# Performance work log

Hardware: AMD Instinct MI355X
Metric: run time of the kernel (lower is better)

The kernel has to match this reference:

```python
import jax, jax.numpy as jnp
import numpy as np

N_HEADS = 16
NEG_INF = -1e9


def _apply_rope(xq, xk, cos, sin):
    # xq, xk: [B, S, H, hd]; cos/sin: [S, hd//2]
    def rot(t):
        B, S, H, hd = t.shape
        t = t.reshape(B, S, H, hd // 2, 2)
        t0, t1 = t[..., 0], t[..., 1]
        c = cos[None, :, None, :]
        s = sin[None, :, None, :]
        o0 = t0 * c - t1 * s
        o1 = t0 * s + t1 * c
        return jnp.stack([o0, o1], axis=-1).reshape(B, S, H, hd)
    return rot(xq), rot(xk)


def setup_inputs() -> dict:
    key = jax.random.key(0)
    ks = jax.random.split(key, 7)
    B, S, D = 2, 2048, 2048
    hd = D // N_HEADS
    return {
        "x": jax.random.normal(ks[0], (B, S, D), dtype=jnp.float32),
        "freqs_cos": jax.random.uniform(ks[1], (S, hd // 2), dtype=jnp.float32),
        "freqs_sin": jax.random.uniform(ks[2], (S, hd // 2), dtype=jnp.float32),
        "wq": jax.random.normal(ks[3], (D, D), dtype=jnp.float32) * 0.02,
        "wk": jax.random.normal(ks[4], (D, D), dtype=jnp.float32) * 0.02,
        "wv": jax.random.normal(ks[5], (D, D), dtype=jnp.float32) * 0.02,
        "wo": jax.random.normal(ks[6], (D, D), dtype=jnp.float32) * 0.02,
    }


def reference(x, freqs_cos, freqs_sin, wq, wk, wv, wo):
    B, S, D = x.shape
    H = N_HEADS
    hd = D // H

    # projections (torch Linear: y = x @ W.T)
    xq = (x @ wq.T).reshape(B, S, H, hd)
    xk = (x @ wk.T).reshape(B, S, H, hd)
    xv = (x @ wv.T).reshape(B, S, H, hd)

    xq, xk = _apply_rope(xq, xk, freqs_cos, freqs_sin)

    # [B, H, S, hd]
    q = xq.transpose(0, 2, 1, 3)
    k = xk.transpose(0, 2, 1, 3)
    v = xv.transpose(0, 2, 1, 3)

    scores = jnp.einsum("bhqd,bhkd->bhqk", q, k) / jnp.sqrt(jnp.float32(hd))
    causal = jnp.triu(jnp.full((S, S), NEG_INF, dtype=scores.dtype), k=1)
    scores = scores + causal[None, None]
    probs = jax.nn.softmax(scores.astype(jnp.float32), axis=-1).astype(q.dtype)

    out = jnp.einsum("bhqk,bhkd->bhqd", probs, v)
    out = out.transpose(0, 2, 1, 3).reshape(B, S, D)
    return out @ wo.T
```

## Files before the change

kernel.cpp:

```cpp
#include <hip/hip_runtime.h>
#include <hip/hip_bf16.h>
#include <math.h>

typedef __attribute__((ext_vector_type(8))) short short8;
typedef __attribute__((ext_vector_type(4))) short short4v;
typedef __attribute__((ext_vector_type(4))) float f32x4;
typedef unsigned short ushort_t;

#define QK_LOG2E_SCALE 0.1275274059009601f

__device__ __forceinline__ ushort_t f2bf(float f) {
    union { float f; unsigned u; } v; v.f = f;
    unsigned r = v.u + 0x7FFF + ((v.u >> 16) & 1);
    return (ushort_t)(r >> 16);
}

__global__ void cvt_all(const float* __restrict__ x,
                        const float* __restrict__ w0, const float* __restrict__ w1,
                        const float* __restrict__ w2, const float* __restrict__ w3,
                        const float* __restrict__ fc, const float* __restrict__ fs,
                        ushort_t* __restrict__ dst, float2* __restrict__ fcs,
                        int md8, int dd8, int npair4) {
    int i = blockIdx.x * blockDim.x + threadIdx.x;
    int stride = gridDim.x * blockDim.x;
    const int total0 = md8 + 4 * dd8;
    const int total = total0 + npair4;
    for (; i < total; i += stride) {
        if (i < total0) {
            const float* src;
            long off;
            if (i < md8) { src = x; off = i; }
            else {
                int j = i - md8;
                int which = j / dd8;
                off = j - (long)which * dd8;
                src = (which == 0) ? w0 : (which == 1) ? w1 : (which == 2) ? w2 : w3;
            }
            const float4* s = reinterpret_cast<const float4*>(src) + off * 2;
            float4 a = s[0], b = s[1];
            short8 o;
            o[0] = (short)f2bf(a.x); o[1] = (short)f2bf(a.y);
            o[2] = (short)f2bf(a.z); o[3] = (short)f2bf(a.w);
            o[4] = (short)f2bf(b.x); o[5] = (short)f2bf(b.y);
            o[6] = (short)f2bf(b.z); o[7] = (short)f2bf(b.w);
            reinterpret_cast<short8*>(dst)[i] = o;
        } else {
            int j = i - total0;
            float4 c4 = reinterpret_cast<const float4*>(fc)[j];
            float4 s4 = reinterpret_cast<const float4*>(fs)[j];
            float2* o = fcs + (long)j * 4;
            o[0] = make_float2(c4.x, s4.x);
            o[1] = make_float2(c4.y, s4.y);
            o[2] = make_float2(c4.z, s4.z);
            o[3] = make_float2(c4.w, s4.w);
        }
    }
}

template<int EPI>
__global__ __launch_bounds__(512, 2) void gemm_wide(const ushort_t* __restrict__ A,
                                                    const ushort_t* __restrict__ Bw,
                                                    void* __restrict__ Cout,
                                                    ushort_t* __restrict__ Vt,
                                                    const float2* __restrict__ fcs,
                                                    int M, int N, int K) {
    extern __shared__ __align__(16) ushort_t lds[];
    ushort_t* As = lds;
    ushort_t* Bs = lds + 16384;
    const int t = threadIdx.x;
    const int wid = t >> 6, lane = t & 63;
    const int wr = wid >> 2, wc = wid & 3;
    const int lr = lane & 15, lg = lane >> 4;

    const int ntc = N >> 8;
    const int nwg = (M >> 7) * ntc;
    const int bid = blockIdx.y * gridDim.x + blockIdx.x;
    const int cpx = nwg >> 3;
    const int swz = (bid & 7) * cpx + (bid >> 3);
    const int m0 = (swz / ntc) * 128, n0 = (swz % ntc) * 256;

    f32x4 acc[4][4] = {};

    const int r0 = t >> 3;
    const int c0 = (t & 7) ^ (r0 & 7);
    const ushort_t* gA = A + (long)(m0 + r0) * K + c0 * 8;
    const ushort_t* gB = Bw + (long)(n0 + r0) * K + c0 * 8;

    int aoffE[2];
    aoffE[0] = lr * 64 + (((0 + lg) ^ (lr & 7)) << 3);
    aoffE[1] = lr * 64 + (((4 + lg) ^ (lr & 7)) << 3);

    const int nt = K >> 6;

#define STAGE_A(X) do { const int p_ = (X) & 1;                                                \
    __builtin_amdgcn_global_load_lds((const __attribute__((address_space(1))) unsigned int*)   \
        (gA + (X) * 64),                                                                       \
        (__attribute__((address_space(3))) unsigned int*)(As + p_ * 8192 + t * 8), 16, 0, 0);  \
    __builtin_amdgcn_global_load_lds((const __attribute__((address_space(1))) unsigned int*)   \
        (gA + (long)64 * K + (X) * 64),                                                        \
        (__attribute__((address_space(3))) unsigned int*)(As + p_ * 8192 + 4096 + t * 8), 16, 0, 0); } while (0)

#define STAGE_B(X) do { const int p_ = (X) & 1;                                                \
    _Pragma("unroll")                                                                          \
    for (int j_ = 0; j_ < 4; ++j_)                                                             \
        __builtin_amdgcn_global_load_lds((const __attribute__((address_space(1))) unsigned int*) \
            (gB + (long)(j_ * 64) * K + (X) * 64),                                             \
            (__attribute__((address_space(3))) unsigned int*)(Bs + p_ * 16384 + j_ * 4096 + t * 8), 16, 0, 0); } while (0)

#define MIDSYNC() do {                                             \
    asm volatile("" ::: "memory");                                 \
    __builtin_amdgcn_s_barrier();                                  \
    asm volatile("s_waitcnt lgkmcnt(0)" ::: "memory");             \
    __builtin_amdgcn_sched_barrier(0); } while (0)

#define ENDBAR() do {                                              \
    asm volatile("" ::: "memory");                                 \
    __builtin_amdgcn_s_barrier(); } while (0)

#define MFMA_Q(BCOL, BR) do {                                      \
    __builtin_amdgcn_s_setprio(1);                                 \
    _Pragma("unroll")                                              \
    for (int ks = 0; ks < 2; ++ks)                                 \
        _Pragma("unroll")                                          \
        for (int m = 0; m < 4; ++m)                                \
            _Pragma("unroll")                                      \
            for (int n = 0; n < 2; ++n)                            \
                acc[m][(BCOL) + n] =                               \
                    __builtin_amdgcn_mfma_f32_16x16x32_bf16(ar[m][ks], (BR)[n][ks], acc[m][(BCOL) + n], 0, 0, 0); \
    __builtin_amdgcn_s_setprio(0); } while (0)

#define KTILE(U, BUF) do {                                                                     \
    const int Asb = (BUF) * 8192 + wr * 4096;                                                  \
    const int Bcb = (BUF) * 16384 + wc * 4096;                                                 \
    _Pragma("unroll")                                                                          \
    for (int m = 0; m < 4; ++m)                                                                \
        _Pragma("unroll")                                                                      \
        for (int ks = 0; ks < 2; ++ks)                                                         \
            ar[m][ks] = *reinterpret_cast<const short8*>(&As[Asb + m * 1024 + aoffE[ks]]);     \
    _Pragma("unroll")                                                                          \
    for (int n = 0; n < 2; ++n)                                                                \
        _Pragma("unroll")                                                                      \
        for (int ks = 0; ks < 2; ++ks)                                                         \
            br0[n][ks] = *reinterpret_cast<const short8*>(&Bs[Bcb + n * 1024 + aoffE[ks]]);    \
    MIDSYNC();                                                                                 \
    MFMA_Q(0, br0);                                                                            \
    ENDBAR();                                                                                  \
    _Pragma("unroll")                                                                          \
    for (int n = 0; n < 2; ++n)                                                                \
        _Pragma("unroll")                                                                      \
        for (int ks = 0; ks < 2; ++ks)                                                         \
            br1[n][ks] = *reinterpret_cast<const short8*>(&Bs[Bcb + 2048 + n * 1024 + aoffE[ks]]); \
    if ((U) + 2 < nt) STAGE_A((U) + 2);                                                        \
    MIDSYNC();                                                                                 \
    MFMA_Q(2, br1);                                                                            \
    if ((U) + 2 < nt) STAGE_B((U) + 2);                                                        \
    asm volatile("" ::: "memory");                                                             \
    if ((U) < nt - 2) {                                                                        \
        asm volatile("s_waitcnt vmcnt(6)" ::: "memory");                                       \
    } else if ((U) == nt - 2) {                                                                \
        asm volatile("s_waitcnt vmcnt(0)" ::: "memory");                                       \
    }                                                                                          \
    __builtin_amdgcn_s_barrier(); } while (0)

    STAGE_A(0); STAGE_B(0); STAGE_A(1); STAGE_B(1);
    asm volatile("s_waitcnt vmcnt(6)" ::: "memory");
    __builtin_amdgcn_s_barrier();

    short8 ar[4][2], br0[2][2], br1[2][2];

    for (int U = 0; U < nt; U += 2) {
        KTILE(U, 0);
        KTILE(U + 1, 1);
    }
#undef KTILE
#undef MFMA_Q
#undef ENDBAR
#undef MIDSYNC
#undef STAGE_A
#undef STAGE_B

    const int S = 2048;
    #pragma unroll
    for (int m = 0; m < 4; ++m) {
        #pragma unroll
        for (int n = 0; n < 4; ++n) {
            const int col = n0 + wc * 64 + n * 16 + lr;
            const int rowb = m0 + wr * 64 + m * 16 + lg * 4;
            if (EPI == 0) {
                #pragma unroll
                for (int r = 0; r < 4; ++r)
                    ((float*)Cout)[(long)(rowb + r) * N + col] = acc[m][n][r];
            } else {
                const int which = col >> 11;
                const int h = (col >> 7) & 15;
                const int d = col & 127;
                const int bb = rowb >> 11;
                const int sb = rowb & 2047;
                if (which == 2) {
                    short4v o;
                    #pragma unroll
                    for (int r = 0; r < 4; ++r) o[r] = (short)f2bf(acc[m][n][r]);
                    *reinterpret_cast<short4v*>(Vt + ((long)(bb * 16 + h) * 128 + d) * S + sb) = o;
                } else {
                    const int i0 = d >> 1;
                    const float qs = (which == 0) ? QK_LOG2E_SCALE : 1.0f;
                    #pragma unroll
                    for (int r = 0; r < 4; ++r) {
                        const int s = sb + r;
                        float v = acc[m][n][r];
                        float p = __shfl_xor(v, 1);
                        float2 cs = fcs[(long)s * 64 + i0];
                        float o = (lr & 1) ? (p * cs.y + v * cs.x) : (v * cs.x - p * cs.y);
                        ((ushort_t*)Cout)[(long)which * M * 2048 +
                                          (((long)(bb * 16 + h)) * 2048 + s) * 128 + d] = f2bf(o * qs);
                    }
                }
            }
        }
    }
}

__global__ __launch_bounds__(256, 3) void attn_kernel(const ushort_t* __restrict__ Qp,
                                                      const ushort_t* __restrict__ Kp,
                                                      const ushort_t* __restrict__ Vtg,
                                                      ushort_t* __restrict__ O,
                                                      int S, int H) {
    __shared__ __align__(16) ushort_t Ks[64 * 128];
    __shared__ __align__(16) ushort_t Vs[128 * 64];
    __shared__ __align__(16) ushort_t Pl[4][16][72];
    const int t = threadIdx.x, wid = t >> 6, lane = t & 63;
    const int lr = lane & 15, lg = lane >> 4;

    const int slot = blockIdx.x;
    const int xcd = slot & 7;
    const int idx = slot >> 3;
    const int bh = xcd + 8 * (idx >> 4);
    const int fold = idx & 15;

    const int b = bh / H, h = bh % H;
    const ushort_t* Qh = Qp + (long)bh * S * 128;
    const ushort_t* Kh = Kp + (long)bh * S * 128;
    const ushort_t* Vth = Vtg + (long)bh * 128 * S;
    const int nq = S / 64;

    const int ksr = t >> 2;
    const int vsr = t & 127;
    const int vsc = (t >> 7) * 32;

    for (int qsel = 0; qsel < 2; ++qsel) {
        const int qt = qsel ? (nq - 1 - fold) : fold;
        const int qb0 = qt * 64;

        const int qrow = qb0 + wid * 16 + lr;
        short8 qf[4];
        #pragma unroll
        for (int kk = 0; kk < 4; ++kk)
            qf[kk] = *reinterpret_cast<const short8*>(Qh + (long)qrow * 128 + kk * 32 + lg * 8);

        f32x4 oacc[8] = {};
        float mrow[4], lsum[4];
        #pragma unroll
        for (int r = 0; r < 4; ++r) { mrow[r] = -INFINITY; lsum[r] = 0.f; }

        const int nkt = qt + 1;

        short8 kreg[4], vreg[4];
        {
            const ushort_t* kgp = Kh + t * 32;
            const ushort_t* vgp = Vth + (long)vsr * S + vsc;
            #pragma unroll
            for (int j = 0; j < 4; ++j) kreg[j] = *reinterpret_cast<const short8*>(kgp + j * 8);
            #pragma unroll
            for (int j = 0; j < 4; ++j) vreg[j] = *reinterpret_cast<const short8*>(vgp + j * 8);
        }

        for (int kt = 0; kt < nkt; ++kt) {
            const int kv0 = kt * 64;
            __syncthreads();
            #pragma unroll
            for (int j = 0; j < 4; ++j)
                *reinterpret_cast<short8*>(&Ks[(ksr << 7) + (((((t & 3) << 2) + j) ^ (ksr & 7)) << 3)]) = kreg[j];
            #pragma unroll
            for (int j = 0; j < 4; ++j)
                *reinterpret_cast<short8*>(&Vs[(vsr << 6) + (((((t >> 7) << 2) + j) ^ (vsr & 7)) << 3)]) = vreg[j];
            __syncthreads();
            if (kt + 1 < nkt) {
                const ushort_t* kgp = Kh + (long)(kv0 + 64) * 128 + t * 32;
                const ushort_t* vgp = Vth + (long)vsr * S + kv0 + 64 + vsc;
                #pragma unroll
                for (int j = 0; j < 4; ++j) kreg[j] = *reinterpret_cast<const short8*>(kgp + j * 8);
                #pragma unroll
                for (int j = 0; j < 4; ++j) vreg[j] = *reinterpret_cast<const short8*>(vgp + j * 8);
            }

            f32x4 sacc[4] = {};
            #pragma unroll
            for (int kk = 0; kk < 4; ++kk) {
                #pragma unroll
                for (int n = 0; n < 4; ++n) {
                    short8 kf = *reinterpret_cast<const short8*>(
                        &Ks[((n * 16 + lr) << 7) + ((((kk << 2) + lg) ^ (lr & 7)) << 3)]);
                    sacc[n] = __builtin_amdgcn_mfma_f32_16x16x32_bf16(qf[kk], kf, sacc[n], 0, 0, 0);
                }
            }
            float sv[4][4];
            if (kt == qt) {
                const int myq = qb0 + wid * 16 + lg * 4;
                #pragma unroll
                for (int n = 0; n < 4; ++n) {
                    int kcol = kv0 + n * 16 + lr;
                    #pragma unroll
                    for (int r = 0; r < 4; ++r)
                        sv[n][r] = (kcol > myq + r) ? -1e9f : sacc[n][r];
                }
            } else {
                #pragma unroll
                for (int n = 0; n < 4; ++n)
                    #pragma unroll
                    for (int r = 0; r < 4; ++r)
                        sv[n][r] = sacc[n][r];
            }
            float alpha[4];
            #pragma unroll
            for (int r = 0; r < 4; ++r) {
                float mx = fmaxf(fmaxf(sv[0][r], sv[1][r]), fmaxf(sv[2][r], sv[3][r]));
                #pragma unroll
                for (int off = 1; off < 16; off <<= 1)
                    mx = fmaxf(mx, __shfl_xor(mx, off));
                float mnew = fmaxf(mrow[r], mx);
                alpha[r] = __builtin_amdgcn_exp2f(mrow[r] - mnew);
                float ts = 0.f;
                #pragma unroll
                for (int n = 0; n < 4; ++n) {
                    float p = __builtin_amdgcn_exp2f(sv[n][r] - mnew);
                    sv[n][r] = p;
                    ts += p;
                }
                #pragma unroll
                for (int off = 1; off < 16; off <<= 1)
                    ts += __shfl_xor(ts, off);
                lsum[r] = lsum[r] * alpha[r] + ts;
                mrow[r] = mnew;
            }
            #pragma unroll
            for (int f = 0; f < 8; ++f)
                #pragma unroll
                for (int r = 0; r < 4; ++r)
                    oacc[f][r] *= alpha[r];
            #pragma unroll
            for (int n = 0; n < 4; ++n)
                #pragma unroll
                for (int r = 0; r < 4; ++r)
                    Pl[wid][lg * 4 + r][n * 16 + lr] = f2bf(sv[n][r]);
            __asm volatile("" ::: "memory");
            short8 pf[2];
            #pragma unroll
            for (int ks = 0; ks < 2; ++ks)
                pf[ks] = *reinterpret_cast<const short8*>(&Pl[wid][lr][ks * 32 + lg * 8]);
            #pragma unroll
            for (int ks = 0; ks < 2; ++ks) {
                #pragma unroll
                for (int f = 0; f < 8; ++f) {
                    short8 vf = *reinterpret_cast<const short8*>(
                        &Vs[((f * 16 + lr) << 6) + ((((ks << 2) + lg) ^ (lr & 7)) << 3)]);
                    oacc[f] = __builtin_amdgcn_mfma_f32_16x16x32_bf16(pf[ks], vf, oacc[f], 0, 0, 0);
                }
            }
        }
        float inv[4];
        #pragma unroll
        for (int r = 0; r < 4; ++r) inv[r] = 1.f / lsum[r];
        ushort_t* Oh = O + (long)b * S * 2048 + h * 128;
        #pragma unroll
        for (int f = 0; f < 8; ++f) {
            #pragma unroll
            for (int r = 0; r < 4; ++r) {
                int row = qb0 + wid * 16 + lg * 4 + r;
                int col = f * 16 + lr;
                Oh[(long)row * 2048 + col] = f2bf(oacc[f][r] * inv[r]);
            }
        }
    }
}

extern "C" void kernel_launch(void* const* d_in, const int* in_sizes, int n_in,
                              void* d_out, int out_size, void* d_ws, size_t ws_size,
                              hipStream_t stream) {
    const float* x  = (const float*)d_in[0];
    const float* fc = (const float*)d_in[1];
    const float* fs = (const float*)d_in[2];
    const float* wq = (const float*)d_in[3];
    const float* wk = (const float*)d_in[4];
    const float* wv = (const float*)d_in[5];
    const float* wo = (const float*)d_in[6];
    float* out = (float*)d_out;

    const int B = 2, S = 2048, D = 2048, H = 16;
    const int M = B * S;
    const size_t MD = (size_t)M * D;
    const size_t DD = (size_t)D * D;

    char* ws = (char*)d_ws;
    ushort_t* xbf = (ushort_t*)ws;
    ushort_t* wqb = (ushort_t*)(ws + MD * 2);
    ushort_t* wob = wqb + 3 * DD;
    ushort_t* qp  = wqb + 4 * DD;
    ushort_t* kp  = qp + MD;
    ushort_t* vtg = kp + MD;
    float2* fcs   = (float2*)(vtg + MD);
    ushort_t* attnb = xbf;

    const int npair4 = S * 64 / 4;
    cvt_all<<<2048, 256, 0, stream>>>(x, wq, wk, wv, wo, fc, fs, xbf, fcs,
                                      (int)(MD / 8), (int)(DD / 8), npair4);

    dim3 gq(6144 / 256, M / 128);
    gemm_wide<1><<<gq, 512, 98304, stream>>>(xbf, wqb, qp, vtg, fcs, M, 3 * D, D);

    const int nblk = (S / 128) * (B * H);
    attn_kernel<<<nblk, 256, 0, stream>>>(qp, kp, vtg, attnb, S, H);

    dim3 gg(D / 256, M / 128);
    gemm_wide<0><<<gg, 512, 98304, stream>>>(attnb, wob, out, nullptr, nullptr, M, D, D);
}
```

Before: 289.7 us.

## Process both folded query tiles in one KV sweep to share K/V loads

The attention kernel used to run two separate passes over K/V, one per folded query tile. It now keeps both tiles' Q fragments and accumulators in registers and makes a single sweep up to the later tile. Each staged K/V block is used for both tiles while the earlier tile is still active, which cuts global loads and LDS staging. The cost is roughly double the accumulator registers, so launch bounds drop from 3 to 2 blocks per SM, lowering occupancy.

```diff
diff --git a/kernel.cpp b/kernel.cpp
--- a/kernel.cpp
+++ b/kernel.cpp
@@ -220,7 +220,7 @@
     }
 }
 
-__global__ __launch_bounds__(256, 3) void attn_kernel(const ushort_t* __restrict__ Qp,
+__global__ __launch_bounds__(256, 2) void attn_kernel(const ushort_t* __restrict__ Qp,
                                                       const ushort_t* __restrict__ Kp,
                                                       const ushort_t* __restrict__ Vtg,
                                                       ushort_t* __restrict__ O,
@@ -242,144 +242,168 @@
     const ushort_t* Kh = Kp + (long)bh * S * 128;
     const ushort_t* Vth = Vtg + (long)bh * 128 * S;
     const int nq = S / 64;
+    const int qt1 = fold, qt2 = nq - 1 - fold;
+    const int qb1 = qt1 * 64, qb2 = qt2 * 64;
 
     const int ksr = t >> 2;
     const int vsr = t & 127;
     const int vsc = (t >> 7) * 32;
 
-    for (int qsel = 0; qsel < 2; ++qsel) {
-        const int qt = qsel ? (nq - 1 - fold) : fold;
-        const int qb0 = qt * 64;
-
-        const int qrow = qb0 + wid * 16 + lr;
-        short8 qf[4];
-        #pragma unroll
-        for (int kk = 0; kk < 4; ++kk)
-            qf[kk] = *reinterpret_cast<const short8*>(Qh + (long)qrow * 128 + kk * 32 + lg * 8);
-
-        f32x4 oacc[8] = {};
-        float mrow[4], lsum[4];
-        #pragma unroll
-        for (int r = 0; r < 4; ++r) { mrow[r] = -INFINITY; lsum[r] = 0.f; }
-
-        const int nkt = qt + 1;
-
-        short8 kreg[4], vreg[4];
-        {
-            const ushort_t* kgp = Kh + t * 32;
-            const ushort_t* vgp = Vth + (long)vsr * S + vsc;
-            #pragma unroll
-            for (int j = 0; j < 4; ++j) kreg[j] = *reinterpret_cast<const short8*>(kgp + j * 8);
-            #pragma unroll
-            for (int j = 0; j < 4; ++j) vreg[j] = *reinterpret_cast<const short8*>(vgp + j * 8);
-        }
-
-        for (int kt = 0; kt < nkt; ++kt) {
-            const int kv0 = kt * 64;
-            __syncthreads();
-            #pragma unroll
-            for (int j = 0; j < 4; ++j)
-                *reinterpret_cast<short8*>(&Ks[(ksr << 7) + (((((t & 3) << 2) + j) ^ (ksr & 7)) << 3)]) = kreg[j];
-            #pragma unroll
-            for (int j = 0; j < 4; ++j)
-                *reinterpret_cast<short8*>(&Vs[(vsr << 6) + (((((t >> 7) << 2) + j) ^ (vsr & 7)) << 3)]) = vreg[j];
-            __syncthreads();
-            if (kt + 1 < nkt) {
-                const ushort_t* kgp = Kh + (long)(kv0 + 64) * 128 + t * 32;
-                const ushort_t* vgp = Vth + (long)vsr * S + kv0 + 64 + vsc;
-                #pragma unroll
-                for (int j = 0; j < 4; ++j) kreg[j] = *reinterpret_cast<const short8*>(kgp + j * 8);
-                #pragma unroll
-                for (int j = 0; j < 4; ++j) vreg[j] = *reinterpret_cast<const short8*>(vgp + j * 8);
-            }
-
-            f32x4 sacc[4] = {};
-            #pragma unroll
-            for (int kk = 0; kk < 4; ++kk) {
-                #pragma unroll
-                for (int n = 0; n < 4; ++n) {
-                    short8 kf = *reinterpret_cast<const short8*>(
-                        &Ks[((n * 16 + lr) << 7) + ((((kk << 2) + lg) ^ (lr & 7)) << 3)]);
-                    sacc[n] = __builtin_amdgcn_mfma_f32_16x16x32_bf16(qf[kk], kf, sacc[n], 0, 0, 0);
-                }
-            }
-            float sv[4][4];
-            if (kt == qt) {
-                const int myq = qb0 + wid * 16 + lg * 4;
-                #pragma unroll
-                for (int n = 0; n < 4; ++n) {
-                    int kcol = kv0 + n * 16 + lr;
-                    #pragma unroll
-                    for (int r = 0; r < 4; ++r)
-                        sv[n][r] = (kcol > myq + r) ? -1e9f : sacc[n][r];
-                }
-            } else {
-                #pragma unroll
-                for (int n = 0; n < 4; ++n)
-                    #pragma unroll
-                    for (int r = 0; r < 4; ++r)
-                        sv[n][r] = sacc[n][r];
-            }
-            float alpha[4];
-            #pragma unroll
-            for (int r = 0; r < 4; ++r) {
-                float mx = fmaxf(fmaxf(sv[0][r], sv[1][r]), fmaxf(sv[2][r], sv[3][r]));
-                #pragma unroll
-                for (int off = 1; off < 16; off <<= 1)
-                    mx = fmaxf(mx, __shfl_xor(mx, off));
-                float mnew = fmaxf(mrow[r], mx);
-                alpha[r] = __builtin_amdgcn_exp2f(mrow[r] - mnew);
-                float ts = 0.f;
-                #pragma unroll
-                for (int n = 0; n < 4; ++n) {
-                    float p = __builtin_amdgcn_exp2f(sv[n][r] - mnew);
-                    sv[n][r] = p;
-                    ts += p;
-                }
-                #pragma unroll
-                for (int off = 1; off < 16; off <<= 1)
-                    ts += __shfl_xor(ts, off);
-                lsum[r] = lsum[r] * alpha[r] + ts;
-                mrow[r] = mnew;
-            }
-            #pragma unroll
-            for (int f = 0; f < 8; ++f)
+    short8 qf1[4], qf2[4];
+    {
+        const int qr1 = qb1 + wid * 16 + lr;
+        const int qr2 = qb2 + wid * 16 + lr;
+        #pragma unroll
+        for (int kk = 0; kk < 4; ++kk) {
+            qf1[kk] = *reinterpret_cast<const short8*>(Qh + (long)qr1 * 128 + kk * 32 + lg * 8);
+            qf2[kk] = *reinterpret_cast<const short8*>(Qh + (long)qr2 * 128 + kk * 32 + lg * 8);
+        }
+    }
+
+    f32x4 oacc1[8] = {}, oacc2[8] = {};
+    float mrow1[4], lsum1[4], mrow2[4], lsum2[4];
+    #pragma unroll
+    for (int r = 0; r < 4; ++r) {
+        mrow1[r] = -INFINITY; lsum1[r] = 0.f;
+        mrow2[r] = -INFINITY; lsum2[r] = 0.f;
+    }
+
+    auto tile_compute = [&](const short8* qf, f32x4* oacc, float* mrow, float* lsum,
+                            int qb0, bool diag, int kv0) {
+        f32x4 sacc[4] = {};
+        #pragma unroll
+        for (int kk = 0; kk < 4; ++kk) {
+            #pragma unroll
+            for (int n = 0; n < 4; ++n) {
+                short8 kf = *reinterpret_cast<const short8*>(
+                    &Ks[((n * 16 + lr) << 7) + ((((kk << 2) + lg) ^ (lr & 7)) << 3)]);
+                sacc[n] = __builtin_amdgcn_mfma_f32_16x16x32_bf16(qf[kk], kf, sacc[n], 0, 0, 0);
+            }
+        }
+        float sv[4][4];
+        if (diag) {
+            const int myq = qb0 + wid * 16 + lg * 4;
+            #pragma unroll
+            for (int n = 0; n < 4; ++n) {
+                int kcol = kv0 + n * 16 + lr;
                 #pragma unroll
                 for (int r = 0; r < 4; ++r)
-                    oacc[f][r] *= alpha[r];
+                    sv[n][r] = (kcol > myq + r) ? -1e9f : sacc[n][r];
+            }
+        } else {
             #pragma unroll
             for (int n = 0; n < 4; ++n)
                 #pragma unroll
                 for (int r = 0; r < 4; ++r)
-                    Pl[wid][lg * 4 + r][n * 16 + lr] = f2bf(sv[n][r]);
-            __asm volatile("" ::: "memory");
-            short8 pf[2];
-            #pragma unroll
-            for (int ks = 0; ks < 2; ++ks)
-                pf[ks] = *reinterpret_cast<const short8*>(&Pl[wid][lr][ks * 32 + lg * 8]);
-            #pragma unroll
-            for (int ks = 0; ks < 2; ++ks) {
-                #pragma unroll
-                for (int f = 0; f < 8; ++f) {
-                    short8 vf = *reinterpret_cast<const short8*>(
-                        &Vs[((f * 16 + lr) << 6) + ((((ks << 2) + lg) ^ (lr & 7)) << 3)]);
-                    oacc[f] = __builtin_amdgcn_mfma_f32_16x16x32_bf16(pf[ks], vf, oacc[f], 0, 0, 0);
-                }
-            }
-        }
+                    sv[n][r] = sacc[n][r];
+        }
+        float alpha[4];
+        #pragma unroll
+        for (int r = 0; r < 4; ++r) {
+            float mx = fmaxf(fmaxf(sv[0][r], sv[1][r]), fmaxf(sv[2][r], sv[3][r]));
+            #pragma unroll
+            for (int off = 1; off < 16; off <<= 1)
+                mx = fmaxf(mx, __shfl_xor(mx, off));
+            float mnew = fmaxf(mrow[r], mx);
+            alpha[r] = __builtin_amdgcn_exp2f(mrow[r] - mnew);
+            float ts = 0.f;
+            #pragma unroll
+            for (int n = 0; n < 4; ++n) {
+                float p = __builtin_amdgcn_exp2f(sv[n][r] - mnew);
+                sv[n][r] = p;
+                ts += p;
+            }
+            #pragma unroll
+            for (int off = 1; off < 16; off <<= 1)
+                ts += __shfl_xor(ts, off);
+            lsum[r] = lsum[r] * alpha[r] + ts;
+            mrow[r] = mnew;
+        }
+        #pragma unroll
+        for (int f = 0; f < 8; ++f)
+            #pragma unroll
+            for (int r = 0; r < 4; ++r)
+                oacc[f][r] *= alpha[r];
+        #pragma unroll
+        for (int n = 0; n < 4; ++n)
+            #pragma unroll
+            for (int r = 0; r < 4; ++r)
+                Pl[wid][lg * 4 + r][n * 16 + lr] = f2bf(sv[n][r]);
+        __asm volatile("" ::: "memory");
+        short8 pf[2];
+        #pragma unroll
+        for (int ks = 0; ks < 2; ++ks)
+            pf[ks] = *reinterpret_cast<const short8*>(&Pl[wid][lr][ks * 32 + lg * 8]);
+        #pragma unroll
+        for (int ks = 0; ks < 2; ++ks) {
+            #pragma unroll
+            for (int f = 0; f < 8; ++f) {
+                short8 vf = *reinterpret_cast<const short8*>(
+                    &Vs[((f * 16 + lr) << 6) + ((((ks << 2) + lg) ^ (lr & 7)) << 3)]);
+                oacc[f] = __builtin_amdgcn_mfma_f32_16x16x32_bf16(pf[ks], vf, oacc[f], 0, 0, 0);
+            }
+        }
+        __asm volatile("" ::: "memory");
+    };
+
+    short8 kreg[4], vreg[4];
+    {
+        const ushort_t* kgp = Kh + t * 32;
+        const ushort_t* vgp = Vth + (long)vsr * S + vsc;
+        #pragma unroll
+        for (int j = 0; j < 4; ++j) kreg[j] = *reinterpret_cast<const short8*>(kgp + j * 8);
+        #pragma unroll
+        for (int j = 0; j < 4; ++j) vreg[j] = *reinterpret_cast<const short8*>(vgp + j * 8);
+    }
+
+    for (int kt = 0; kt <= qt2; ++kt) {
+        const int kv0 = kt * 64;
+        __syncthreads();
+        #pragma unroll
+        for (int j = 0; j < 4; ++j)
+            *reinterpret_cast<short8*>(&Ks[(ksr << 7) + (((((t & 3) << 2) + j) ^ (ksr & 7)) << 3)]) = kreg[j];
+        #pragma unroll
+        for (int j = 0; j < 4; ++j)
+            *reinterpret_cast<short8*>(&Vs[(vsr << 6) + (((((t >> 7) << 2) + j) ^ (vsr & 7)) << 3)]) = vreg[j];
+        __syncthreads();
+        if (kt < qt2) {
+            const ushort_t* kgp = Kh + (long)(kv0 + 64) * 128 + t * 32;
+            const ushort_t* vgp = Vth + (long)vsr * S + kv0 + 64 + vsc;
+            #pragma unroll
+            for (int j = 0; j < 4; ++j) kreg[j] = *reinterpret_cast<const short8*>(kgp + j * 8);
+            #pragma unroll
+            for (int j = 0; j < 4; ++j) vreg[j] = *reinterpret_cast<const short8*>(vgp + j * 8);
+        }
+
+        tile_compute(qf2, oacc2, mrow2, lsum2, qb2, kt == qt2, kv0);
+        if (kt <= qt1)
+            tile_compute(qf1, oacc1, mrow1, lsum1, qb1, kt == qt1, kv0);
+    }
+
+    ushort_t* Oh = O + (long)b * S * 2048 + h * 128;
+    {
         float inv[4];
         #pragma unroll
-        for (int r = 0; r < 4; ++r) inv[r] = 1.f / lsum[r];
-        ushort_t* Oh = O + (long)b * S * 2048 + h * 128;
-        #pragma unroll
-        for (int f = 0; f < 8; ++f) {
+        for (int r = 0; r < 4; ++r) inv[r] = 1.f / lsum1[r];
+        #pragma unroll
+        for (int f = 0; f < 8; ++f)
             #pragma unroll
             for (int r = 0; r < 4; ++r) {
-                int row = qb0 + wid * 16 + lg * 4 + r;
-                int col = f * 16 + lr;
-                Oh[(long)row * 2048 + col] = f2bf(oacc[f][r] * inv[r]);
-            }
-        }
+                int row = qb1 + wid * 16 + lg * 4 + r;
+                Oh[(long)row * 2048 + f * 16 + lr] = f2bf(oacc1[f][r] * inv[r]);
+            }
+    }
+    {
+        float inv[4];
+        #pragma unroll
+        for (int r = 0; r < 4; ++r) inv[r] = 1.f / lsum2[r];
+        #pragma unroll
+        for (int f = 0; f < 8; ++f)
+            #pragma unroll
+            for (int r = 0; r < 4; ++r) {
+                int row = qb2 + wid * 16 + lg * 4 + r;
+                Oh[(long)row * 2048 + f * 16 + lr] = f2bf(oacc2[f][r] * inv[r]);
+            }
     }
 }
 
```

Measured after the change: 267.6 us. 7.6% less time.
